# Kernel tuning notes

Measured on AMD Instinct MI355X. Metric: run time of the kernel, lower is better.

The kernel has to match this reference:

```python
import jax, jax.numpy as jnp
import numpy as np

EPS = 1e-5


def _bn_relu(x, gamma, beta):
    # x: (B, S, K, C); BatchNorm2d in train mode -> stats over (B, S, K) per channel
    mean = jnp.mean(x, axis=(0, 1, 2), keepdims=True)
    var = jnp.var(x, axis=(0, 1, 2), keepdims=True)
    return jax.nn.relu((x - mean) * jax.lax.rsqrt(var + EPS) * gamma + beta)


def setup_inputs() -> dict:
    key = jax.random.key(0)
    ks = jax.random.split(key, 8)
    B, N, D = 16, 4096, 64
    npoint, nsample = 1024, 32
    mlp = [64, 64, 128]
    inp = {
        "xyz": jax.random.normal(ks[0], (B, N, 3), dtype=jnp.float32),
        "points": jax.random.normal(ks[1], (B, N, D), dtype=jnp.float32),
        "fps_idx": jax.random.randint(ks[2], (B, npoint), 0, N, dtype=jnp.int32),
    }
    last = D + 3
    for i, out_c in enumerate(mlp):
        inp[f"w{i}"] = jax.random.normal(ks[3 + i], (out_c, last), dtype=jnp.float32) * 0.05
        inp[f"b{i}"] = jnp.zeros((out_c,), dtype=jnp.float32)
        inp[f"g{i}"] = jnp.ones((out_c,), dtype=jnp.float32)
        inp[f"be{i}"] = jnp.zeros((out_c,), dtype=jnp.float32)
        last = out_c
    return inp


def reference(xyz, points, fps_idx, w0, b0, g0, be0, w1, b1, g1, be1, w2, b2, g2, be2):
    # xyz: (B, N, 3); points: (B, N, D); fps_idx: (B, S)
    nsample = 32
    gather = jax.vmap(lambda pts, i: pts[i])  # per-batch fancy gather

    new_xyz = gather(xyz, fps_idx)  # (B, S, 3)

    # square_distance(new_xyz, xyz): (B, S, N)
    dist = (
        -2.0 * jnp.einsum("bsc,bnc->bsn", new_xyz, xyz)
        + jnp.sum(new_xyz * new_xyz, -1)[..., None]
        + jnp.sum(xyz * xyz, -1)[:, None, :]
    )
    _, idx = jax.lax.top_k(-dist, nsample)  # (B, S, K) nearest neighbors

    grouped_xyz = gather(xyz, idx)  # (B, S, K, 3)
    grouped_xyz_norm = grouped_xyz - new_xyz[:, :, None, :]
    grouped_points = gather(points, idx)  # (B, S, K, D)
    new_points = jnp.concatenate([grouped_xyz_norm, grouped_points], axis=-1)  # (B,S,K,3+D)

    # 1x1 Conv2d == per-point linear; channels-last for efficiency
    for w, b, g, be in ((w0, b0, g0, be0), (w1, b1, g1, be1), (w2, b2, g2, be2)):
        new_points = _bn_relu(jnp.einsum("bskc,oc->bsko", new_points, w) + b, g, be)

    new_points = jnp.max(new_points, axis=2)  # max over nsample -> (B, S, C_out)
    return new_xyz, new_points
```

## Files before the change

### kernel.cpp

```cpp
#include <hip/hip_runtime.h>
#include <hip/hip_bf16.h>


typedef __attribute__((ext_vector_type(8))) short short8;
typedef __attribute__((ext_vector_type(4))) float float4v;

constexpr int BB = 16, NN = 4096, SS = 1024, DD = 64, KK = 32;
constexpr int PP = BB * SS * KK;
constexpr int NG = BB * SS;
constexpr float EPSF = 1e-5f;
constexpr int CAND_MAX = 640;
constexpr int QPB = 8;

constexpr int WS_IDX   = 0;
constexpr int WS_NXYZ  = PP / 2;
constexpr int WS_W0PK  = WS_NXYZ + NG*3;
constexpr int WS_W1PK  = WS_W0PK + 3072;
constexpr int WS_W2PK  = WS_W1PK + 2048;
constexpr int WS_W1PKD = WS_W2PK + 4096;
constexpr int WS_W2PKD = WS_W1PKD + 4096;
constexpr int WS_SUMS  = WS_W2PKD + 8192;
constexpr int WS_SCALE = WS_SUMS + 512;
constexpr int WS_H1    = WS_SCALE + 512;
constexpr int WS_H2    = WS_H1 + PP*32;
constexpr int WS_END   = WS_H2 + PP*32;
constexpr size_t WS_FAST_BYTES = (size_t)WS_END * 4;

__device__ __forceinline__ unsigned rtne16(float x) {
    unsigned b = __float_as_uint(x);
    return (b + 0x7fffu + ((b >> 16) & 1u)) >> 16;
}
__device__ __forceinline__ unsigned rtneb(float r) {
    unsigned b = __float_as_uint(r);
    return b + 0x7fffu + ((b >> 16) & 1u);
}
__device__ __forceinline__ unsigned pk2r(unsigned a, unsigned b) {
    return __builtin_amdgcn_perm(a, b, 0x03020706u);
}
__device__ __forceinline__ unsigned pk2f(float a, float b) {
    return pk2r(__float_as_uint(a), __float_as_uint(b));
}
__device__ __forceinline__ unsigned bnpack(unsigned u, float sce, float sfe,
                                           float sco, float sfo) {
    float fe = __uint_as_float(u << 16);
    float fo = __uint_as_float(u & 0xffff0000u);
    float ze = fmaxf(fmaf(fe, sce, sfe), 0.f);
    float zo = fmaxf(fmaf(fo, sco, sfo), 0.f);
    return pk2r(rtneb(ze), rtneb(zo));
}

union UF { uint4 u; short8 s; };
__device__ __forceinline__ short8 ldw(const uint4* __restrict__ p, int idx) {
    UF u; u.u = p[idx]; return u.s;
}

#define LDS_SYNC() asm volatile("s_waitcnt lgkmcnt(0)" ::: "memory")

__global__ void k_prep(const float* __restrict__ w0, const float* __restrict__ w1,
                       const float* __restrict__ w2, float* __restrict__ ws) {
    const int t = threadIdx.x;
    ushort* w0pk = (ushort*)(ws + WS_W0PK);
    for (int i = t; i < 6144; i += 256) {
        int j = i & 7, l = (i >> 3) & 63, Ks = (i >> 9) % 3, Nt = i / 1536;
        int o = Nt*16 + (l & 15);
        int k = Ks*32 + (l >> 4)*8 + j;
        float v = 0.f;
        if (k < 64)      v = w0[o*67 + 3 + k];
        else if (k < 67) v = w0[o*67 + (k - 64)];
        else if (k < 70) v = w0[o*67 + (k - 67)];
        w0pk[i] = (ushort)rtne16(v);
    }
    ushort* w1pk = (ushort*)(ws + WS_W1PK);
    for (int i = t; i < 4096; i += 256) {
        int j = i & 7, l = (i >> 3) & 63, Ks = (i >> 9) & 1, Nt = i >> 10;
        int o = Nt*16 + (l & 15);
        int k = Ks*32 + (l >> 4)*8 + j;
        w1pk[i] = (ushort)rtne16(w1[o*64 + k]);
    }
    ushort* w2pk = (ushort*)(ws + WS_W2PK);
    for (int i = t; i < 8192; i += 256) {
        int j = i & 7, l = (i >> 3) & 63, Ks = (i >> 9) & 1, Nt = i >> 10;
        int o = Nt*16 + (l & 15);
        int k = Ks*32 + (l >> 4)*8 + j;
        w2pk[i] = (ushort)rtne16(w2[o*64 + k]);
    }
    ushort* w1pd = (ushort*)(ws + WS_W1PKD);
    for (int i = t; i < 8192; i += 256) {
        int j = i & 7, l = (i >> 3) & 63, Ks = (i >> 9) & 3, Nt = i >> 11;
        int o = Nt*16 + (l & 15);
        int c = (Ks*32 + (l >> 4)*8 + j) >> 1;
        w1pd[i] = (ushort)rtne16(w1[o*64 + c]);
    }
    ushort* w2pd = (ushort*)(ws + WS_W2PKD);
    for (int i = t; i < 16384; i += 256) {
        int j = i & 7, l = (i >> 3) & 63, Ks = (i >> 9) & 3, Nt = i >> 11;
        int o = Nt*16 + (l & 15);
        int c = (Ks*32 + (l >> 4)*8 + j) >> 1;
        w2pd[i] = (ushort)rtne16(w2[o*64 + c]);
    }
    for (int i = t; i < 512; i += 256) ws[WS_SUMS + i] = 0.f;
}

__global__ __launch_bounds__(512, 2) void k_select(
    const float* __restrict__ xyz, const int* __restrict__ fps,
    float* __restrict__ out_xyz, float* __restrict__ ws)
{
    __shared__ float sxy[2*NN];
    __shared__ float szz[NN];
    __shared__ unsigned cbk[QPB][CAND_MAX];
    __shared__ ushort  cbi[QPB][CAND_MAX];
    const int tid = threadIdx.x;
    const int qb = blockIdx.x * QPB;
    const int b  = qb >> 10;
    const float* xb = xyz + (long)b * NN * 3;
    for (int i = tid; i < NN; i += 512) {
        sxy[2*i]   = xb[i*3 + 0];
        sxy[2*i+1] = xb[i*3 + 1];
        szz[i]     = xb[i*3 + 2];
    }
    __syncthreads();

    const int wave = tid >> 6, lane = tid & 63;
    const int q = qb + wave;
    const int nq = fps[q];
    const float qx = sxy[2*nq], qy = sxy[2*nq+1], qz = szz[nq];
    const float qw = __fadd_rn(__fadd_rn(__fmul_rn(qx,qx), __fmul_rn(qy,qy)), __fmul_rn(qz,qz));

    float* nxyz = ws + WS_NXYZ;
    unsigned short* idx_ws = (unsigned short*)ws;
    if (lane < 3) {
        float v = (lane == 0) ? qx : ((lane == 1) ? qy : qz);
        out_xyz[q*3 + lane] = v;
        nxyz[q*3 + lane] = v;
    }

    unsigned key[64];
    unsigned lmin = 0xFFFFFFFFu, lmax = 0u;
    #pragma unroll
    for (int i = 0; i < 64; ++i) {
        const int n = i*64 + lane;
        const float px = sxy[2*n], py = sxy[2*n+1], pz = szz[n];
        const float pw = __fadd_rn(__fadd_rn(__fmul_rn(px,px), __fmul_rn(py,py)), __fmul_rn(pz,pz));
        float dot = fmaf(qx, px, 0.f);
        dot = fmaf(qy, py, dot);
        dot = fmaf(qz, pz, dot);
        float d = __fadd_rn(__fadd_rn(__fmul_rn(-2.0f, dot), qw), pw);
        unsigned u = __float_as_uint(d);
        unsigned k = u ^ (unsigned)(((int)u >> 31) | 0x80000000);
        key[i] = k;
        lmin = min(lmin, k); lmax = max(lmax, k);
    }
    unsigned gmin = lmin, gmax = lmax, Bv = lmin;
    #pragma unroll
    for (int off = 32; off > 0; off >>= 1) {
        gmin = min(gmin, (unsigned)__shfl_xor((int)gmin, off));
        gmax = max(gmax, (unsigned)__shfl_xor((int)gmax, off));
        Bv   = max(Bv,   (unsigned)__shfl_xor((int)Bv,   off));
    }

    const unsigned long long lmask = (1ull << lane) - 1ull;
    unsigned* ckw = cbk[wave];
    ushort*   ciw = cbi[wave];

    int cnt = 0;
    #pragma unroll
    for (int i = 0; i < 64; ++i) {
        bool pr = key[i] <= Bv;
        unsigned long long m = __ballot(pr);
        int pos = cnt + (int)__popcll(m & lmask);
        if (pr && pos < CAND_MAX) {
            ckw[pos] = key[i];
            ciw[pos] = (ushort)(i*64 + lane);
        }
        cnt += (int)__popcll(m);
    }
    const int base = q * KK;

    if (cnt <= CAND_MAX) {
        LDS_SYNC();
        unsigned cr[10]; ushort ir[10];
        #pragma unroll
        for (int r = 0; r < 10; ++r) {
            int j = r*64 + lane;
            bool v = j < cnt;
            cr[r] = v ? ckw[j] : 0xFFFFFFFFu;
            ir[r] = v ? ciw[j] : (ushort)0;
        }
        unsigned lo = gmin, hi = Bv;
        while (lo < hi) {
            unsigned mid = lo + ((hi - lo) >> 1);
            int c = 0;
            #pragma unroll
            for (int r = 0; r < 10; ++r)
                c += (int)__popcll(__ballot(cr[r] <= mid));
            if (c >= 32) hi = mid; else lo = mid + 1;
        }
        const unsigned T = lo;

        int c2 = 0;
        #pragma unroll
        for (int r = 0; r < 10; ++r) {
            bool pr = cr[r] < T;
            unsigned long long m = __ballot(pr);
            if (pr) idx_ws[base + c2 + (int)__popcll(m & lmask)] = ir[r];
            c2 += (int)__popcll(m);
        }
        #pragma unroll
        for (int r = 0; r < 10; ++r) {
            bool pr = cr[r] == T;
            unsigned long long m = __ballot(pr);
            int pos = c2 + (int)__popcll(m & lmask);
            if (pr && pos < KK) idx_ws[base + pos] = ir[r];
            c2 += (int)__popcll(m);
        }
    } else {
        unsigned lo = gmin, hi = gmax;
        while (lo < hi) {
            unsigned mid = lo + ((hi - lo) >> 1);
            int c = 0;
            #pragma unroll
            for (int i = 0; i < 64; ++i)
                c += (int)__popcll(__ballot(key[i] <= mid));
            if (c >= 32) hi = mid; else lo = mid + 1;
        }
        const unsigned T = lo;
        int c2 = 0;
        #pragma unroll
        for (int i = 0; i < 64; ++i) {
            bool pr = key[i] < T;
            unsigned long long m = __ballot(pr);
            if (pr) idx_ws[base + c2 + (int)__popcll(m & lmask)] = (ushort)(i*64 + lane);
            c2 += (int)__popcll(m);
        }
        #pragma unroll
        for (int i = 0; i < 64; ++i) {
            bool pr = key[i] == T;
            unsigned long long m = __ballot(pr);
            int pos = c2 + (int)__popcll(m & lmask);
            if (pr && pos < KK) idx_ws[base + pos] = (ushort)(i*64 + lane);
            c2 += (int)__popcll(m);
        }
    }
}


__global__ __launch_bounds__(256, 2) void k_g1(
    const float* __restrict__ xyz, const float* __restrict__ pts,
    const float* __restrict__ b0, float* __restrict__ ws,
    ushort* __restrict__ h1)
{
    __shared__ float rbuf[4][128];
    const int tid = threadIdx.x;
    const int wv = tid >> 6, l = tid & 63, ln = l & 15, q8 = l >> 4;

    const ushort* idxw = (const ushort*)ws;
    const float* nxyz = ws + WS_NXYZ;
    float* sums = ws + WS_SUMS;
    const uint4* w0f = (const uint4*)(ws + WS_W0PK);

    short8 w0r[12];
    #pragma unroll
    for (int t = 0; t < 12; ++t) w0r[t] = ldw(w0f, t*64 + l);
    float b0v[4];
    #pragma unroll
    for (int n = 0; n < 4; ++n) b0v[n] = b0[n*16 + ln];

    float s[4] = {0,0,0,0}, sq[4] = {0,0,0,0};
    const int gbase = blockIdx.x*4 + wv;

    for (int it = 0; it < 4; ++it) {
        const int g = gbase + it*4096;
        const float nqx = nxyz[g*3+0], nqy = nxyz[g*3+1], nqz = nxyz[g*3+2];

        short8 a1[2][3];
        #pragma unroll
        for (int Mt = 0; Mt < 2; ++Mt) {
            int nb = idxw[g*32 + Mt*16 + ln];
            int row = (g >> 10)*NN + nb;
            const float* p = pts + row*64 + q8*8;
            float4 f0 = *(const float4*)p;
            float4 f1 = *(const float4*)(p + 4);
            float4 f2 = *(const float4*)(p + 32);
            float4 f3 = *(const float4*)(p + 36);
            UF t0, t1;
            t0.u.x = pk2f(f0.x, f0.y); t0.u.y = pk2f(f0.z, f0.w);
            t0.u.z = pk2f(f1.x, f1.y); t0.u.w = pk2f(f1.z, f1.w);
            a1[Mt][0] = t0.s;
            t1.u.x = pk2f(f2.x, f2.y); t1.u.y = pk2f(f2.z, f2.w);
            t1.u.z = pk2f(f3.x, f3.y); t1.u.w = pk2f(f3.z, f3.w);
            a1[Mt][1] = t1.s;
            UF x; x.u = make_uint4(0,0,0,0);
            if (q8 == 0) {
                float vx = xyz[row*3+0] - nqx;
                float vy = xyz[row*3+1] - nqy;
                float vz = xyz[row*3+2] - nqz;
                unsigned bx = __float_as_uint(vx), by = __float_as_uint(vy), bz = __float_as_uint(vz);
                float rx = vx - __uint_as_float(bx & 0xffff0000u);
                float ry = vy - __uint_as_float(by & 0xffff0000u);
                float rz = vz - __uint_as_float(bz & 0xffff0000u);
                x.u.x = pk2r(bx, by);
                x.u.y = pk2r(bz, rtneb(rx));
                x.u.z = pk2r(rtneb(ry), rtneb(rz));
            }
            a1[Mt][2] = x.s;
        }

        float4v acc[2][4];
        #pragma unroll
        for (int Mt = 0; Mt < 2; ++Mt)
            #pragma unroll
            for (int Nt = 0; Nt < 4; ++Nt)
                acc[Mt][Nt] = (float4v){b0v[Nt], b0v[Nt], b0v[Nt], b0v[Nt]};
        #pragma unroll
        for (int Ks = 0; Ks < 3; ++Ks)
            #pragma unroll
            for (int Nt = 0; Nt < 4; ++Nt)
                #pragma unroll
                for (int Mt = 0; Mt < 2; ++Mt)
                    acc[Mt][Nt] = __builtin_amdgcn_mfma_f32_16x16x32_bf16(
                        a1[Mt][Ks], w0r[Nt*3 + Ks], acc[Mt][Nt], 0, 0, 0);

        #pragma unroll
        for (int Mt = 0; Mt < 2; ++Mt)
            #pragma unroll
            for (int Nt = 0; Nt < 4; ++Nt)
                #pragma unroll
                for (int r = 0; r < 4; ++r) {
                    float h = acc[Mt][Nt][r];
                    s[Nt] += h; sq[Nt] += h*h;
                    h1[(g*32 + Mt*16 + q8*4 + r)*64 + Nt*16 + ln] = (ushort)rtne16(h);
                }
    }

    #pragma unroll
    for (int t = 0; t < 4; ++t) {
        float a = s[t], b = sq[t];
        a += __shfl_xor(a, 16); a += __shfl_xor(a, 32);
        b += __shfl_xor(b, 16); b += __shfl_xor(b, 32);
        if (l < 16) { rbuf[wv][t*16 + l] = a; rbuf[wv][64 + t*16 + l] = b; }
    }
    __syncthreads();
    if (wv == 0 && l < 16) {
        #pragma unroll
        for (int t = 0; t < 4; ++t) {
            float a = rbuf[0][t*16+l] + rbuf[1][t*16+l] + rbuf[2][t*16+l] + rbuf[3][t*16+l];
            float b = rbuf[0][64+t*16+l] + rbuf[1][64+t*16+l] + rbuf[2][64+t*16+l] + rbuf[3][64+t*16+l];
            atomicAdd(&sums[t*16 + l], a);
            atomicAdd(&sums[64 + t*16 + l], b);
        }
    }
}

__global__ __launch_bounds__(256, 2) void k_g2(
    const float* __restrict__ b1, float* __restrict__ ws,
    const ushort* __restrict__ h1, ushort* __restrict__ h2)
{
    __shared__ float rbuf[4][128];
    const int tid = threadIdx.x;
    const int wv = tid >> 6, l = tid & 63, ln = l & 15, q8 = l >> 4;

    const float* scl = ws + WS_SCALE;
    float* sums = ws + WS_SUMS;
    const uint4* w1f = (const uint4*)(ws + WS_W1PK);

    float b1v[4];
    #pragma unroll
    for (int n = 0; n < 4; ++n) b1v[n] = b1[n*16 + ln];
    float4 sc[2][2], sf[2][2];
    #pragma unroll
    for (int Ks = 0; Ks < 2; ++Ks) {
        sc[Ks][0] = *(const float4*)&scl[Ks*32 + q8*8];
        sc[Ks][1] = *(const float4*)&scl[Ks*32 + q8*8 + 4];
        sf[Ks][0] = *(const float4*)&scl[64 + Ks*32 + q8*8];
        sf[Ks][1] = *(const float4*)&scl[64 + Ks*32 + q8*8 + 4];
    }

    float s[4] = {0,0,0,0}, sq[4] = {0,0,0,0};
    const int gbase = blockIdx.x*4 + wv;

    for (int it = 0; it < 4; ++it) {
        const int g = gbase + it*4096;

        short8 a[2][2];
        #pragma unroll
        for (int Mt = 0; Mt < 2; ++Mt)
            #pragma unroll
            for (int Ks = 0; Ks < 2; ++Ks) {
                uint4 hv = *(const uint4*)&h1[(g*32 + Mt*16 + ln)*64 + Ks*32 + q8*8];
                UF t;
                t.u.x = bnpack(hv.x, sc[Ks][0].x, sf[Ks][0].x, sc[Ks][0].y, sf[Ks][0].y);
                t.u.y = bnpack(hv.y, sc[Ks][0].z, sf[Ks][0].z, sc[Ks][0].w, sf[Ks][0].w);
                t.u.z = bnpack(hv.z, sc[Ks][1].x, sf[Ks][1].x, sc[Ks][1].y, sf[Ks][1].y);
                t.u.w = bnpack(hv.w, sc[Ks][1].z, sf[Ks][1].z, sc[Ks][1].w, sf[Ks][1].w);
                a[Mt][Ks] = t.s;
            }

        float4v acc[2][4];
        #pragma unroll
        for (int Mt = 0; Mt < 2; ++Mt)
            #pragma unroll
            for (int Nt = 0; Nt < 4; ++Nt)
                acc[Mt][Nt] = (float4v){b1v[Nt], b1v[Nt], b1v[Nt], b1v[Nt]};
        #pragma unroll
        for (int Ks = 0; Ks < 2; ++Ks)
            #pragma unroll
            for (int Nt = 0; Nt < 4; ++Nt) {
                short8 bf = ldw(w1f, (Nt*2 + Ks)*64 + l);
                #pragma unroll
                for (int Mt = 0; Mt < 2; ++Mt)
                    acc[Mt][Nt] = __builtin_amdgcn_mfma_f32_16x16x32_bf16(
                        a[Mt][Ks], bf, acc[Mt][Nt], 0, 0, 0);
            }

        #pragma unroll
        for (int Mt = 0; Mt < 2; ++Mt)
            #pragma unroll
            for (int Nt = 0; Nt < 4; ++Nt)
                #pragma unroll
                for (int r = 0; r < 4; ++r) {
                    float h = acc[Mt][Nt][r];
                    s[Nt] += h; sq[Nt] += h*h;
                    h2[(g*32 + Mt*16 + q8*4 + r)*64 + Nt*16 + ln] = (ushort)rtne16(h);
                }
    }

    #pragma unroll
    for (int t = 0; t < 4; ++t) {
        float a = s[t], b = sq[t];
        a += __shfl_xor(a, 16); a += __shfl_xor(a, 32);
        b += __shfl_xor(b, 16); b += __shfl_xor(b, 32);
        if (l < 16) { rbuf[wv][t*16 + l] = a; rbuf[wv][64 + t*16 + l] = b; }
    }
    __syncthreads();
    if (wv == 0 && l < 16) {
        #pragma unroll
        for (int t = 0; t < 4; ++t) {
            float a = rbuf[0][t*16+l] + rbuf[1][t*16+l] + rbuf[2][t*16+l] + rbuf[3][t*16+l];
            float b = rbuf[0][64+t*16+l] + rbuf[1][64+t*16+l] + rbuf[2][64+t*16+l] + rbuf[3][64+t*16+l];
            atomicAdd(&sums[128 + t*16 + l], a);
            atomicAdd(&sums[192 + t*16 + l], b);
        }
    }
}

__global__ __launch_bounds__(256, 2) void k_g3(
    const float* __restrict__ b2, const float* __restrict__ g2,
    float* __restrict__ ws, const ushort* __restrict__ h2,
    float* __restrict__ out_pts)
{
    __shared__ float rbuf[4][256];
    const int tid = threadIdx.x;
    const int wv = tid >> 6, l = tid & 63, ln = l & 15, q8 = l >> 4;

    const float* scl = ws + WS_SCALE;
    float* sums = ws + WS_SUMS;
    const uint4* w2f = (const uint4*)(ws + WS_W2PK);

    float b2v[8], g2v[8];
    #pragma unroll
    for (int n = 0; n < 8; ++n) { b2v[n] = b2[n*16 + ln]; g2v[n] = g2[n*16 + ln]; }
    float4 sc[2][2], sf[2][2];
    #pragma unroll
    for (int Ks = 0; Ks < 2; ++Ks) {
        sc[Ks][0] = *(const float4*)&scl[128 + Ks*32 + q8*8];
        sc[Ks][1] = *(const float4*)&scl[128 + Ks*32 + q8*8 + 4];
        sf[Ks][0] = *(const float4*)&scl[192 + Ks*32 + q8*8];
        sf[Ks][1] = *(const float4*)&scl[192 + Ks*32 + q8*8 + 4];
    }

    float s[8] = {0,0,0,0,0,0,0,0}, sq[8] = {0,0,0,0,0,0,0,0};
    const int gbase = blockIdx.x*4 + wv;

    for (int it = 0; it < 4; ++it) {
        const int g = gbase + it*4096;

        short8 a[2][2];
        #pragma unroll
        for (int Mt = 0; Mt < 2; ++Mt)
            #pragma unroll
            for (int Ks = 0; Ks < 2; ++Ks) {
                uint4 hv = *(const uint4*)&h2[(g*32 + Mt*16 + ln)*64 + Ks*32 + q8*8];
                UF t;
                t.u.x = bnpack(hv.x, sc[Ks][0].x, sf[Ks][0].x, sc[Ks][0].y, sf[Ks][0].y);
                t.u.y = bnpack(hv.y, sc[Ks][0].z, sf[Ks][0].z, sc[Ks][0].w, sf[Ks][0].w);
                t.u.z = bnpack(hv.z, sc[Ks][1].x, sf[Ks][1].x, sc[Ks][1].y, sf[Ks][1].y);
                t.u.w = bnpack(hv.w, sc[Ks][1].z, sf[Ks][1].z, sc[Ks][1].w, sf[Ks][1].w);
                a[Mt][Ks] = t.s;
            }

        float4v acc[2][8];
        #pragma unroll
        for (int Mt = 0; Mt < 2; ++Mt)
            #pragma unroll
            for (int Nt = 0; Nt < 8; ++Nt)
                acc[Mt][Nt] = (float4v){b2v[Nt], b2v[Nt], b2v[Nt], b2v[Nt]};
        #pragma unroll
        for (int Ks = 0; Ks < 2; ++Ks)
            #pragma unroll
            for (int Nt = 0; Nt < 8; ++Nt) {
                short8 bf = ldw(w2f, (Nt*2 + Ks)*64 + l);
                #pragma unroll
                for (int Mt = 0; Mt < 2; ++Mt)
                    acc[Mt][Nt] = __builtin_amdgcn_mfma_f32_16x16x32_bf16(
                        a[Mt][Ks], bf, acc[Mt][Nt], 0, 0, 0);
            }

        float mm[8];
        #pragma unroll
        for (int Nt = 0; Nt < 8; ++Nt) {
            const bool pos = g2v[Nt] >= 0.f;
            float m = acc[0][Nt][0];
            #pragma unroll
            for (int Mt = 0; Mt < 2; ++Mt)
                #pragma unroll
                for (int r = 0; r < 4; ++r) {
                    float h = acc[Mt][Nt][r];
                    s[Nt] += h; sq[Nt] += h*h;
                    if (!(Mt == 0 && r == 0))
                        m = pos ? fmaxf(m, h) : fminf(m, h);
                }
            float o = __shfl_xor(m, 16); m = pos ? fmaxf(m, o) : fminf(m, o);
            o = __shfl_xor(m, 32);       m = pos ? fmaxf(m, o) : fminf(m, o);
            mm[Nt] = m;
        }
        if (l < 16) {
            #pragma unroll
            for (int Nt = 0; Nt < 8; ++Nt)
                out_pts[(long)g*128 + Nt*16 + l] = mm[Nt];
        }
    }

    #pragma unroll
    for (int t = 0; t < 8; ++t) {
        float a = s[t], b = sq[t];
        a += __shfl_xor(a, 16); a += __shfl_xor(a, 32);
        b += __shfl_xor(b, 16); b += __shfl_xor(b, 32);
        if (l < 16) { rbuf[wv][t*16 + l] = a; rbuf[wv][128 + t*16 + l] = b; }
    }
    __syncthreads();
    if (wv == 0 && l < 16) {
        #pragma unroll
        for (int t = 0; t < 8; ++t) {
            float a = rbuf[0][t*16+l] + rbuf[1][t*16+l] + rbuf[2][t*16+l] + rbuf[3][t*16+l];
            float b = rbuf[0][128+t*16+l] + rbuf[1][128+t*16+l] + rbuf[2][128+t*16+l] + rbuf[3][128+t*16+l];
            atomicAdd(&sums[256 + t*16 + l], a);
            atomicAdd(&sums[384 + t*16 + l], b);
        }
    }
}

template<int STAGE>
__global__ __launch_bounds__(256, 2) void k_passF(
    const float* __restrict__ xyz, const float* __restrict__ pts,
    const float* __restrict__ b0, const float* __restrict__ b1,
    const float* __restrict__ b2, const float* __restrict__ g2,
    float* __restrict__ ws, float* __restrict__ out_pts)
{
    __shared__ __align__(16) ushort zb[(STAGE >= 2) ? 4*32*136 : 8];
    const int tid = threadIdx.x;
    const int wv = tid >> 6, l = tid & 63, ln = l & 15, q8 = l >> 4;
    ushort* zw = &zb[(STAGE >= 2) ? wv*32*136 : 0];

    const ushort* idxw = (const ushort*)ws;
    const float* nxyz = ws + WS_NXYZ;
    const float* scl  = ws + WS_SCALE;
    float*       sums = ws + WS_SUMS;
    const uint4* w0f = (const uint4*)(ws + WS_W0PK);
    const uint4* w1f = (const uint4*)(ws + WS_W1PKD);
    const uint4* w2f = (const uint4*)(ws + WS_W2PKD);

    float b0v[4];
    #pragma unroll
    for (int n = 0; n < 4; ++n) b0v[n] = b0[n*16 + ln];
    float sc1v[4], sf1v[4], b1v[4];
    if constexpr (STAGE >= 2) {
        #pragma unroll
        for (int n = 0; n < 4; ++n) {
            sc1v[n] = scl[n*16 + ln]; sf1v[n] = scl[64 + n*16 + ln];
            b1v[n] = b1[n*16 + ln];
        }
    }
    float sc2v[4], sf2v[4], b2v[8], g2v[8];
    if constexpr (STAGE >= 3) {
        #pragma unroll
        for (int n = 0; n < 4; ++n) {
            sc2v[n] = scl[128 + n*16 + ln]; sf2v[n] = scl[192 + n*16 + ln];
        }
        #pragma unroll
        for (int n = 0; n < 8; ++n) { b2v[n] = b2[n*16 + ln]; g2v[n] = g2[n*16 + ln]; }
    }

    float s[8] = {0,0,0,0,0,0,0,0}, sq[8] = {0,0,0,0,0,0,0,0};

    for (int g = blockIdx.x*4 + wv; g < NG; g += 4096) {
        const float nqx = nxyz[g*3+0], nqy = nxyz[g*3+1], nqz = nxyz[g*3+2];
        short8 a1[2][3];
        #pragma unroll
        for (int Mt = 0; Mt < 2; ++Mt) {
            int nb = idxw[g*32 + Mt*16 + ln];
            int row = (g >> 10)*NN + nb;
            const float* p = pts + row*64 + q8*8;
            float4 f0 = *(const float4*)p, f1 = *(const float4*)(p + 4);
            float4 f2 = *(const float4*)(p + 32), f3 = *(const float4*)(p + 36);
            UF t0, t1;
            t0.u.x = pk2f(f0.x, f0.y); t0.u.y = pk2f(f0.z, f0.w);
            t0.u.z = pk2f(f1.x, f1.y); t0.u.w = pk2f(f1.z, f1.w);
            a1[Mt][0] = t0.s;
            t1.u.x = pk2f(f2.x, f2.y); t1.u.y = pk2f(f2.z, f2.w);
            t1.u.z = pk2f(f3.x, f3.y); t1.u.w = pk2f(f3.z, f3.w);
            a1[Mt][1] = t1.s;
            UF x; x.u = make_uint4(0,0,0,0);
            if (q8 == 0) {
                float vx = xyz[row*3+0] - nqx, vy = xyz[row*3+1] - nqy, vz = xyz[row*3+2] - nqz;
                unsigned bx = __float_as_uint(vx), by = __float_as_uint(vy), bz = __float_as_uint(vz);
                float rx = vx - __uint_as_float(bx & 0xffff0000u);
                float ry = vy - __uint_as_float(by & 0xffff0000u);
                float rz = vz - __uint_as_float(bz & 0xffff0000u);
                x.u.x = pk2r(bx, by);
                x.u.y = pk2r(bz, rtneb(rx));
                x.u.z = pk2r(rtneb(ry), rtneb(rz));
            }
            a1[Mt][2] = x.s;
        }

        float4v acc1[2][4];
        #pragma unroll
        for (int Mt = 0; Mt < 2; ++Mt)
            #pragma unroll
            for (int Nt = 0; Nt < 4; ++Nt)
                acc1[Mt][Nt] = (float4v){b0v[Nt], b0v[Nt], b0v[Nt], b0v[Nt]};
        #pragma unroll
        for (int Ks = 0; Ks < 3; ++Ks)
            #pragma unroll
            for (int Nt = 0; Nt < 4; ++Nt) {
                short8 bf = ldw(w0f, (Nt*3 + Ks)*64 + l);
                #pragma unroll
                for (int Mt = 0; Mt < 2; ++Mt)
                    acc1[Mt][Nt] = __builtin_amdgcn_mfma_f32_16x16x32_bf16(
                        a1[Mt][Ks], bf, acc1[Mt][Nt], 0, 0, 0);
            }

        if constexpr (STAGE == 1) {
            #pragma unroll
            for (int Nt = 0; Nt < 4; ++Nt)
                #pragma unroll
                for (int Mt = 0; Mt < 2; ++Mt)
                    #pragma unroll
                    for (int r = 0; r < 4; ++r) {
                        float h = acc1[Mt][Nt][r];
                        s[Nt] += h; sq[Nt] += h*h;
                    }
        }

        if constexpr (STAGE >= 2) {
            #pragma unroll
            for (int Mt = 0; Mt < 2; ++Mt)
                #pragma unroll
                for (int Nt = 0; Nt < 4; ++Nt)
                    #pragma unroll
                    for (int r = 0; r < 4; ++r) {
                        float z = fmaxf(fmaf(acc1[Mt][Nt][r], sc1v[Nt], sf1v[Nt]), 0.f);
                        unsigned zu = __float_as_uint(z);
                        float rr = z - __uint_as_float(zu & 0xffff0000u);
                        *(unsigned*)&zw[(Mt*16 + q8*4 + r)*136 + 2*(Nt*16 + ln)] = pk2r(zu, rtneb(rr));
                    }
            LDS_SYNC();

            float4v acc2[2][4];
            #pragma unroll
            for (int Mt = 0; Mt < 2; ++Mt)
                #pragma unroll
                for (int Nt = 0; Nt < 4; ++Nt)
                    acc2[Mt][Nt] = (float4v){b1v[Nt], b1v[Nt], b1v[Nt], b1v[Nt]};
            #pragma unroll
            for (int Ks = 0; Ks < 4; ++Ks) {
                short8 a2[2];
                #pragma unroll
                for (int Mt = 0; Mt < 2; ++Mt)
                    a2[Mt] = *(const short8*)&zw[(Mt*16 + ln)*136 + Ks*32 + q8*8];
                #pragma unroll
                for (int Nt = 0; Nt < 4; ++Nt) {
                    short8 bf = ldw(w1f, (Nt*4 + Ks)*64 + l);
                    #pragma unroll
                    for (int Mt = 0; Mt < 2; ++Mt)
                        acc2[Mt][Nt] = __builtin_amdgcn_mfma_f32_16x16x32_bf16(
                            a2[Mt], bf, acc2[Mt][Nt], 0, 0, 0);
                }
            }

            if constexpr (STAGE == 2) {
                #pragma unroll
                for (int Nt = 0; Nt < 4; ++Nt)
                    #pragma unroll
                    for (int Mt = 0; Mt < 2; ++Mt)
                        #pragma unroll
                        for (int r = 0; r < 4; ++r) {
                            float h = acc2[Mt][Nt][r];
                            s[Nt] += h; sq[Nt] += h*h;
                        }
            }

            if constexpr (STAGE == 3) {
                LDS_SYNC();
                #pragma unroll
                for (int Mt = 0; Mt < 2; ++Mt)
                    #pragma unroll
                    for (int Nt = 0; Nt < 4; ++Nt)
                        #pragma unroll
                        for (int r = 0; r < 4; ++r) {
                            float z = fmaxf(fmaf(acc2[Mt][Nt][r], sc2v[Nt], sf2v[Nt]), 0.f);
                            unsigned zu = __float_as_uint(z);
                            float rr = z - __uint_as_float(zu & 0xffff0000u);
                            *(unsigned*)&zw[(Mt*16 + q8*4 + r)*136 + 2*(Nt*16 + ln)] = pk2r(zu, rtneb(rr));
                        }
                LDS_SYNC();

                float4v acc3[2][8];
                #pragma unroll
                for (int Mt = 0; Mt < 2; ++Mt)
                    #pragma unroll
                    for (int Nt = 0; Nt < 8; ++Nt)
                        acc3[Mt][Nt] = (float4v){b2v[Nt], b2v[Nt], b2v[Nt], b2v[Nt]};
                #pragma unroll
                for (int Ks = 0; Ks < 4; ++Ks) {
                    short8 a2[2];
                    #pragma unroll
                    for (int Mt = 0; Mt < 2; ++Mt)
                        a2[Mt] = *(const short8*)&zw[(Mt*16 + ln)*136 + Ks*32 + q8*8];
                    #pragma unroll
                    for (int Nt = 0; Nt < 8; ++Nt) {
                        short8 bf = ldw(w2f, (Nt*4 + Ks)*64 + l);
                        #pragma unroll
                        for (int Mt = 0; Mt < 2; ++Mt)
                            acc3[Mt][Nt] = __builtin_amdgcn_mfma_f32_16x16x32_bf16(
                                a2[Mt], bf, acc3[Mt][Nt], 0, 0, 0);
                    }
                }

                float mm[8];
                #pragma unroll
                for (int Nt = 0; Nt < 8; ++Nt) {
                    const bool pos = g2v[Nt] >= 0.f;
                    float m = acc3[0][Nt][0];
                    #pragma unroll
                    for (int Mt = 0; Mt < 2; ++Mt)
                        #pragma unroll
                        for (int r = 0; r < 4; ++r) {
                            float h = acc3[Mt][Nt][r];
                            s[Nt] += h; sq[Nt] += h*h;
                            if (!(Mt == 0 && r == 0))
                                m = pos ? fmaxf(m, h) : fminf(m, h);
                        }
                    float o = __shfl_xor(m, 16); m = pos ? fmaxf(m, o) : fminf(m, o);
                    o = __shfl_xor(m, 32);       m = pos ? fmaxf(m, o) : fminf(m, o);
                    mm[Nt] = m;
                }
                if (l < 16) {
                    #pragma unroll
                    for (int Nt = 0; Nt < 8; ++Nt)
                        out_pts[(long)g*128 + Nt*16 + l] = mm[Nt];
                }
            }
        }
    }

    constexpr int NT = (STAGE == 3) ? 8 : 4;
    constexpr int soff = (STAGE == 1) ? 0 : (STAGE == 2) ? 128 : 256;
    constexpr int qoff = (STAGE == 1) ? 64 : (STAGE == 2) ? 192 : 384;
    #pragma unroll
    for (int t = 0; t < NT; ++t) {
        float a = s[t], b = sq[t];
        a += __shfl_xor(a, 16); a += __shfl_xor(a, 32);
        b += __shfl_xor(b, 16); b += __shfl_xor(b, 32);
        if (l < 16) {
            atomicAdd(&sums[soff + t*16 + l], a);
            atomicAdd(&sums[qoff + t*16 + l], b);
        }
    }
}

__global__ void k_fin(const float* __restrict__ sums, const float* __restrict__ g,
                      const float* __restrict__ be, float* __restrict__ scl,
                      int sum_off, int sq_off, int sc_off, int sh_off, int C)
{
    int c = threadIdx.x;
    if (c < C) {
        float mean = sums[sum_off + c] * (1.0f / PP);
        float var  = sums[sq_off + c] * (1.0f / PP) - mean * mean;
        float s = g[c] * rsqrtf(var + EPSF);
        scl[sc_off + c] = s;
        scl[sh_off + c] = be[c] - mean * s;
    }
}

__global__ void k_bnmax(float* __restrict__ op, const float* __restrict__ scl) {
    int i = blockIdx.x * 256 + threadIdx.x;
    int c = i & 127;
    float sc = scl[256 + c], sf = scl[384 + c];
    op[i] = fmaxf(fmaf(op[i], sc, sf), 0.f);
}

extern "C" void kernel_launch(void* const* d_in, const int* in_sizes, int n_in,
                              void* d_out, int out_size, void* d_ws, size_t ws_size,
                              hipStream_t stream) {
    const float* xyz = (const float*)d_in[0];
    const float* pts = (const float*)d_in[1];
    const int*   fps = (const int*)d_in[2];
    const float* w0  = (const float*)d_in[3];
    const float* b0  = (const float*)d_in[4];
    const float* g0  = (const float*)d_in[5];
    const float* be0 = (const float*)d_in[6];
    const float* w1  = (const float*)d_in[7];
    const float* b1  = (const float*)d_in[8];
    const float* g1  = (const float*)d_in[9];
    const float* be1 = (const float*)d_in[10];
    const float* w2  = (const float*)d_in[11];
    const float* b2  = (const float*)d_in[12];
    const float* g2  = (const float*)d_in[13];
    const float* be2 = (const float*)d_in[14];

    float* ws = (float*)d_ws;
    float* out_xyz = (float*)d_out;
    float* out_pts = (float*)d_out + NG * 3;

    k_prep<<<1, 256, 0, stream>>>(w0, w1, w2, ws);
    k_select<<<NG / QPB, 512, 0, stream>>>(xyz, fps, out_xyz, ws);

    if (ws_size >= WS_FAST_BYTES) {
        ushort* h1 = (ushort*)(ws + WS_H1);
        ushort* h2 = (ushort*)(ws + WS_H2);
        k_g1<<<1024, 256, 0, stream>>>(xyz, pts, b0, ws, h1);
        k_fin<<<1, 128, 0, stream>>>(ws + WS_SUMS, g0, be0, ws + WS_SCALE, 0, 64, 0, 64, 64);
        k_g2<<<1024, 256, 0, stream>>>(b1, ws, h1, h2);
        k_fin<<<1, 128, 0, stream>>>(ws + WS_SUMS, g1, be1, ws + WS_SCALE, 128, 192, 128, 192, 64);
        k_g3<<<1024, 256, 0, stream>>>(b2, g2, ws, h2, out_pts);
        k_fin<<<1, 128, 0, stream>>>(ws + WS_SUMS, g2, be2, ws + WS_SCALE, 256, 384, 256, 384, 128);
    } else {
        k_passF<1><<<1024, 256, 0, stream>>>(xyz, pts, b0, b1, b2, g2, ws, out_pts);
        k_fin<<<1, 128, 0, stream>>>(ws + WS_SUMS, g0, be0, ws + WS_SCALE, 0, 64, 0, 64, 64);
        k_passF<2><<<1024, 256, 0, stream>>>(xyz, pts, b0, b1, b2, g2, ws, out_pts);
        k_fin<<<1, 128, 0, stream>>>(ws + WS_SUMS, g1, be1, ws + WS_SCALE, 128, 192, 128, 192, 64);
        k_passF<3><<<1024, 256, 0, stream>>>(xyz, pts, b0, b1, b2, g2, ws, out_pts);
        k_fin<<<1, 128, 0, stream>>>(ws + WS_SUMS, g2, be2, ws + WS_SCALE, 256, 384, 256, 384, 128);
    }
    k_bnmax<<<NG * 128 / 256, 256, 0, stream>>>(out_pts, ws + WS_SCALE);
}
```

Baseline: 387.4 us.

## Recompute distance keys from global xyz instead of caching in registers and LDS

The kNN select kernel no longer stages the batch's xyz in shared memory or holds 64 keys per lane in registers. Each pass recomputes the squared-distance key straight from global memory, and the candidate buffer keeps only indices. Launch bounds are raised from 2 to 8 blocks per CU to raise occupancy now that LDS and register use are lower. In exchange, the kernel reads global memory repeatedly with a stride-3 access pattern and redoes the arithmetic in every pass, with many passes in the fallback binary search.

New measurement: 484.6 us. 25.1% more time.

```diff
diff --git a/kernel.cpp b/kernel.cpp
--- a/kernel.cpp
+++ b/kernel.cpp
@@ -101,29 +101,20 @@
     for (int i = t; i < 512; i += 256) ws[WS_SUMS + i] = 0.f;
 }
 
-__global__ __launch_bounds__(512, 2) void k_select(
+__global__ __launch_bounds__(512, 8) void k_select(
     const float* __restrict__ xyz, const int* __restrict__ fps,
     float* __restrict__ out_xyz, float* __restrict__ ws)
 {
-    __shared__ float sxy[2*NN];
-    __shared__ float szz[NN];
-    __shared__ unsigned cbk[QPB][CAND_MAX];
-    __shared__ ushort  cbi[QPB][CAND_MAX];
+    __shared__ ushort cbi[QPB][CAND_MAX];
     const int tid = threadIdx.x;
     const int qb = blockIdx.x * QPB;
     const int b  = qb >> 10;
-    const float* xb = xyz + (long)b * NN * 3;
-    for (int i = tid; i < NN; i += 512) {
-        sxy[2*i]   = xb[i*3 + 0];
-        sxy[2*i+1] = xb[i*3 + 1];
-        szz[i]     = xb[i*3 + 2];
-    }
-    __syncthreads();
+    const float* __restrict__ xb = xyz + (long)b * NN * 3;
 
     const int wave = tid >> 6, lane = tid & 63;
     const int q = qb + wave;
     const int nq = fps[q];
-    const float qx = sxy[2*nq], qy = sxy[2*nq+1], qz = szz[nq];
+    const float qx = xb[nq*3 + 0], qy = xb[nq*3 + 1], qz = xb[nq*3 + 2];
     const float qw = __fadd_rn(__fadd_rn(__fmul_rn(qx,qx), __fmul_rn(qy,qy)), __fmul_rn(qz,qz));
 
     float* nxyz = ws + WS_NXYZ;
@@ -134,20 +125,21 @@
         nxyz[q*3 + lane] = v;
     }
 
-    unsigned key[64];
-    unsigned lmin = 0xFFFFFFFFu, lmax = 0u;
-    #pragma unroll
-    for (int i = 0; i < 64; ++i) {
-        const int n = i*64 + lane;
-        const float px = sxy[2*n], py = sxy[2*n+1], pz = szz[n];
-        const float pw = __fadd_rn(__fadd_rn(__fmul_rn(px,px), __fmul_rn(py,py)), __fmul_rn(pz,pz));
+    auto keyAt = [&](int n) -> unsigned {
+        float px = xb[n*3 + 0], py = xb[n*3 + 1], pz = xb[n*3 + 2];
+        float pw = __fadd_rn(__fadd_rn(__fmul_rn(px,px), __fmul_rn(py,py)), __fmul_rn(pz,pz));
         float dot = fmaf(qx, px, 0.f);
         dot = fmaf(qy, py, dot);
         dot = fmaf(qz, pz, dot);
         float d = __fadd_rn(__fadd_rn(__fmul_rn(-2.0f, dot), qw), pw);
         unsigned u = __float_as_uint(d);
-        unsigned k = u ^ (unsigned)(((int)u >> 31) | 0x80000000);
-        key[i] = k;
+        return u ^ (unsigned)(((int)u >> 31) | 0x80000000);
+    };
+
+    unsigned lmin = 0xFFFFFFFFu, lmax = 0u;
+    #pragma unroll 8
+    for (int i = 0; i < 64; ++i) {
+        unsigned k = keyAt(i*64 + lane);
         lmin = min(lmin, k); lmax = max(lmax, k);
     }
     unsigned gmin = lmin, gmax = lmax, Bv = lmin;
@@ -159,19 +151,15 @@
     }
 
     const unsigned long long lmask = (1ull << lane) - 1ull;
-    unsigned* ckw = cbk[wave];
-    ushort*   ciw = cbi[wave];
+    ushort* ciw = cbi[wave];
 
     int cnt = 0;
-    #pragma unroll
+    #pragma unroll 8
     for (int i = 0; i < 64; ++i) {
-        bool pr = key[i] <= Bv;
+        bool pr = keyAt(i*64 + lane) <= Bv;
         unsigned long long m = __ballot(pr);
         int pos = cnt + (int)__popcll(m & lmask);
-        if (pr && pos < CAND_MAX) {
-            ckw[pos] = key[i];
-            ciw[pos] = (ushort)(i*64 + lane);
-        }
+        if (pr && pos < CAND_MAX) ciw[pos] = (ushort)(i*64 + lane);
         cnt += (int)__popcll(m);
     }
     const int base = q * KK;
@@ -183,8 +171,9 @@
         for (int r = 0; r < 10; ++r) {
             int j = r*64 + lane;
             bool v = j < cnt;
-            cr[r] = v ? ckw[j] : 0xFFFFFFFFu;
-            ir[r] = v ? ciw[j] : (ushort)0;
+            ushort idx = v ? ciw[j] : (ushort)0;
+            ir[r] = idx;
+            cr[r] = v ? keyAt(idx) : 0xFFFFFFFFu;
         }
         unsigned lo = gmin, hi = Bv;
         while (lo < hi) {
@@ -218,23 +207,23 @@
         while (lo < hi) {
             unsigned mid = lo + ((hi - lo) >> 1);
             int c = 0;
-            #pragma unroll
+            #pragma unroll 4
             for (int i = 0; i < 64; ++i)
-                c += (int)__popcll(__ballot(key[i] <= mid));
+                c += (int)__popcll(__ballot(keyAt(i*64 + lane) <= mid));
             if (c >= 32) hi = mid; else lo = mid + 1;
         }
         const unsigned T = lo;
         int c2 = 0;
-        #pragma unroll
+        #pragma unroll 4
         for (int i = 0; i < 64; ++i) {
-            bool pr = key[i] < T;
+            bool pr = keyAt(i*64 + lane) < T;
             unsigned long long m = __ballot(pr);
             if (pr) idx_ws[base + c2 + (int)__popcll(m & lmask)] = (ushort)(i*64 + lane);
             c2 += (int)__popcll(m);
         }
-        #pragma unroll
+        #pragma unroll 4
         for (int i = 0; i < 64; ++i) {
-            bool pr = key[i] == T;
+            bool pr = keyAt(i*64 + lane) == T;
             unsigned long long m = __ballot(pr);
             int pos = c2 + (int)__popcll(m & lmask);
             if (pr && pos < KK) idx_ws[base + pos] = (ushort)(i*64 + lane);
```
